# Kernel tuning notes

Hardware: AMD Instinct MI355X
Metric: run time of the kernel (lower is better)

## Reference

```python
import jax, jax.numpy as jnp
import numpy as np

B, S, E, H = 2, 2048, 1024, 16
DK = E // H


def setup_inputs() -> dict:
    key = jax.random.key(0)
    ks = jax.random.split(key, 8)
    scale = 1.0 / np.sqrt(E)
    inp = {
        "query": jax.random.normal(ks[0], (B, S, E), jnp.float32),
        "key": jax.random.normal(ks[1], (B, S, E), jnp.float32),
        "value": jax.random.normal(ks[2], (B, S, E), jnp.float32),
        # causal mask: True = masked out (upper triangle)
        "attn_mask": jnp.triu(jnp.ones((S, S), jnp.bool_), k=1),
        "Wq": jax.random.normal(ks[3], (E, E), jnp.float32) * scale,
        "bq": jnp.zeros((E,), jnp.float32),
        "Wk": jax.random.normal(ks[4], (E, E), jnp.float32) * scale,
        "bk": jnp.zeros((E,), jnp.float32),
        "Wv": jax.random.normal(ks[5], (E, E), jnp.float32) * scale,
        "bv": jnp.zeros((E,), jnp.float32),
        "Wo": jax.random.normal(ks[6], (E, E), jnp.float32) * scale,
        "bo": jnp.zeros((E,), jnp.float32),
    }
    return inp


def reference(query, key, value, attn_mask, Wq, bq, Wk, bk, Wv, bv, Wo, bo):
    bs = query.shape[0]
    # QKV projections, split heads: [B,S,E] -> [B,H,S,DK]
    def proj(x, W, b):
        y = jnp.einsum('bse,ef->bsf', x, W) + b
        return y.reshape(bs, -1, H, DK).transpose(0, 2, 1, 3)

    q = proj(query, Wq, bq)
    k = proj(key, Wk, bk)
    v = proj(value, Wv, bv)

    # scaled dot-product attention with additive -1e9 mask fill
    scores = jnp.einsum('bhqd,bhkd->bhqk', q, k) / np.sqrt(DK).astype(jnp.float32)
    scores = jnp.where(attn_mask[None, None, :, :], jnp.float32(-1e9), scores)
    attn = jax.nn.softmax(scores, axis=-1)
    ctx = jnp.einsum('bhqk,bhkd->bhqd', attn, v)  # [B,H,S,DK]

    concat = ctx.transpose(0, 2, 1, 3).reshape(bs, -1, E)  # [B,S,E]
    return jnp.einsum('bse,ef->bsf', concat, Wo) + bo
```

## Files before the change

### kernel.cpp

```cpp
#include <hip/hip_runtime.h>
#include <hip/hip_bf16.h>

typedef __attribute__((ext_vector_type(8))) short bf16x8;
typedef __attribute__((ext_vector_type(4))) float f32x4;

constexpr int Bc = 2, Sc = 2048, Ec = 1024, Hc = 16, DKc = 64;

__device__ __forceinline__ unsigned short f2b(float f) {
    union { float f; unsigned u; } v; v.f = f;
    unsigned u = v.u;
    return (unsigned short)((u + 0x7FFFu + ((u >> 16) & 1u)) >> 16);
}
__device__ __forceinline__ unsigned short f2bn(float f) {
    return __bfloat16_as_ushort(__float2bfloat16(f));
}
__device__ __forceinline__ float b2f(unsigned short h) {
    union { unsigned u; float f; } v; v.u = ((unsigned)h) << 16;
    return v.f;
}

#define GLOAD16(ldsp, gp)                                                                  \
    __builtin_amdgcn_global_load_lds((const __attribute__((address_space(1))) void*)(gp),  \
                                     (__attribute__((address_space(3))) void*)(ldsp),      \
                                     16, 0, 0)

#define ASM_VM6 asm volatile("s_waitcnt vmcnt(6)" ::: "memory")
#define ASM_VM4 asm volatile("s_waitcnt vmcnt(4)" ::: "memory")
#define ASM_VM0 asm volatile("s_waitcnt vmcnt(0)" ::: "memory")
#define ASM_LG0 asm volatile("s_waitcnt lgkmcnt(0)" ::: "memory")
#define ASM_BAR asm volatile("s_barrier" ::: "memory")

__global__ __launch_bounds__(256) void conv_w(
    const float* __restrict__ Wq, const float* __restrict__ Wk,
    const float* __restrict__ Wv, const float* __restrict__ Wo,
    unsigned short* __restrict__ Wt)
{
    const int z = blockIdx.z;
    const float* W = (z == 0) ? Wq : (z == 1) ? Wk : (z == 2) ? Wv : Wo;
    unsigned short* O = Wt + (size_t)z * 1048576;
    __shared__ unsigned short T[64][65];
    const int k0 = blockIdx.y * 64, n0 = blockIdx.x * 64;
    const int tx = threadIdx.x & 15, ty = threadIdx.x >> 4;
    #pragma unroll
    for (int p = 0; p < 4; p++) {
        float4 v = *(const float4*)&W[(size_t)(k0 + ty + 16 * p) * 1024 + n0 + 4 * tx];
        T[ty + 16 * p][4 * tx + 0] = f2b(v.x);
        T[ty + 16 * p][4 * tx + 1] = f2b(v.y);
        T[ty + 16 * p][4 * tx + 2] = f2b(v.z);
        T[ty + 16 * p][4 * tx + 3] = f2b(v.w);
    }
    __syncthreads();
    #pragma unroll
    for (int p = 0; p < 4; p++) {
        ushort4 o;
        o.x = T[4 * tx + 0][ty + 16 * p];
        o.y = T[4 * tx + 1][ty + 16 * p];
        o.z = T[4 * tx + 2][ty + 16 * p];
        o.w = T[4 * tx + 3][ty + 16 * p];
        *(ushort4*)&O[(size_t)(n0 + ty + 16 * p) * 1024 + k0 + 4 * tx] = o;
    }
}

__global__ __launch_bounds__(256, 2) void gemm_qkv(
    const float* __restrict__ Xq, const float* __restrict__ Xk, const float* __restrict__ Xv,
    const unsigned short* __restrict__ Wt,
    const float* __restrict__ bq, const float* __restrict__ bk, const float* __restrict__ bv,
    unsigned short* __restrict__ Qw, unsigned short* __restrict__ Kw,
    unsigned short* __restrict__ Vt)
{
    const int wgid = blockIdx.x;
    const int xcd = wgid & 7, slot = wgid >> 3;
    const int y = xcd + 8 * (slot & 3);
    const int xz = slot >> 2;
    const int x = xz & 7, z = xz >> 3;

    const float* Ag = (z == 0) ? Xq : (z == 1) ? Xk : Xv;
    const unsigned short* Bg = Wt + (size_t)z * 1048576;
    const float* bias = (z == 0) ? bq : (z == 1) ? bk : bv;

    __shared__ __align__(16) float SA[2][4096];
    __shared__ __align__(16) unsigned short SB[2][4096];

    const int tid = threadIdx.x;
    const int m0 = y * 128, n0 = x * 128;
    const int lane = tid & 63, c = lane & 15, g = lane >> 4;
    const int w = tid >> 6;
    const int wr = (w >> 1) * 64, wc = (w & 1) * 64;
    const int cc = c & 7;
    const int arow = lane >> 3;
    const int achk = ((lane & 7) ^ arow) << 4;
    const int lr = lane >> 2;
    const int lcs = ((lane & 3) ^ ((lane >> 3) & 3)) * 8;

#define QKV_STAGE(buf, kk)                                                                 \
    _Pragma("unroll")                                                                      \
    for (int i = 0; i < 4; i++)                                                            \
        GLOAD16((char*)SA[buf] + i * 4096 + w * 1024,                                      \
                (const char*)Ag + (size_t)(m0 + 32 * i + 8 * w + arow) * 4096 +            \
                (size_t)(kk) * 4 + achk);                                                  \
    _Pragma("unroll")                                                                      \
    for (int i = 0; i < 2; i++) {                                                          \
        const int rb = 32 * w + 16 * i;                                                    \
        GLOAD16(SB[buf] + rb * 32, Bg + (size_t)(n0 + rb + lr) * 1024 + (kk) + lcs);       \
    }

    f32x4 acc[4][4] = {};
    QKV_STAGE(0, 0)
    QKV_STAGE(1, 32)
    for (int t = 0; t < 32; t++) {
        const int cur = t & 1;
        if (t < 31) { ASM_VM6; } else { ASM_VM0; }
        ASM_BAR;
        f32x4 afr[4][2];
        bf16x8 b[4];
        #pragma unroll
        for (int m = 0; m < 4; m++) {
            const char* ab = (const char*)SA[cur] + (wr + 16 * m + c) * 128;
            afr[m][0] = *(const f32x4*)(ab + (((2 * g) ^ cc) << 4));
            afr[m][1] = *(const f32x4*)(ab + (((2 * g + 1) ^ cc) << 4));
        }
        #pragma unroll
        for (int n = 0; n < 4; n++)
            b[n] = *(const bf16x8*)((const char*)SB[cur] +
                   (wc + 16 * n + c) * 64 + ((g ^ ((c >> 1) & 3)) << 4));
        ASM_LG0;
        ASM_BAR;
        if (t + 2 < 32) { QKV_STAGE(cur, (t + 2) * 32) }
        bf16x8 a[4];
        #pragma unroll
        for (int m = 0; m < 4; m++) {
            bf16x8 av;
            av[0] = (short)f2bn(afr[m][0][0]); av[1] = (short)f2bn(afr[m][0][1]);
            av[2] = (short)f2bn(afr[m][0][2]); av[3] = (short)f2bn(afr[m][0][3]);
            av[4] = (short)f2bn(afr[m][1][0]); av[5] = (short)f2bn(afr[m][1][1]);
            av[6] = (short)f2bn(afr[m][1][2]); av[7] = (short)f2bn(afr[m][1][3]);
            a[m] = av;
        }
        __builtin_amdgcn_s_setprio(1);
        #pragma unroll
        for (int m = 0; m < 4; m++)
            #pragma unroll
            for (int n = 0; n < 4; n++)
                acc[m][n] = __builtin_amdgcn_mfma_f32_16x16x32_bf16(a[m], b[n], acc[m][n], 0, 0, 0);
        __builtin_amdgcn_s_setprio(0);
    }
#undef QKV_STAGE

    if (z == 2) {
        unsigned short* Tr = (unsigned short*)&SA[0][0];
        ASM_BAR;
        #pragma unroll
        for (int n = 0; n < 4; n++) {
            const int dl = wc + n * 16 + c;
            const float bv_ = bias[n0 + dl];
            #pragma unroll
            for (int m = 0; m < 4; m++) {
                const int sl = wr + m * 16 + 4 * g;
                ushort4 pw;
                pw.x = f2bn(acc[m][n][0] + bv_);
                pw.y = f2bn(acc[m][n][1] + bv_);
                pw.z = f2bn(acc[m][n][2] + bv_);
                pw.w = f2bn(acc[m][n][3] + bv_);
                const int sc = (sl >> 2) ^ (dl & 7);
                *(ushort4*)&Tr[dl * 128 + sc * 4] = pw;
            }
        }
        ASM_BAR;
        #pragma unroll
        for (int it = 0; it < 16; it++) {
            const int idx = it * 256 + tid;
            const int dl = idx >> 5;
            const int sc0 = idx & 31;
            const int sc = sc0 ^ (dl & 7);
            const ushort4 pw = *(const ushort4*)&Tr[dl * 128 + sc * 4];
            const int gn = n0 + dl;
            const int h = gn >> 6, d = gn & 63;
            const int gm = m0 + sc0 * 4;
            const int bb = gm >> 11, s = gm & 2047;
            *(ushort4*)&Vt[((size_t)(bb * Hc + h) * DKc + d) * Sc + s] = pw;
        }
    } else {
        #pragma unroll
        for (int n = 0; n < 4; n++) {
            const int gn = n0 + wc + n * 16 + c;
            const float bv_ = bias[gn];
            const int h = gn >> 6, d = gn & 63;
            #pragma unroll
            for (int m = 0; m < 4; m++) {
                #pragma unroll
                for (int r = 0; r < 4; r++) {
                    const int gm = m0 + wr + m * 16 + 4 * g + r;
                    const int bb = gm >> 11, s = gm & 2047;
                    const float val = acc[m][n][r] + bv_;
                    if (z == 0)
                        Qw[((size_t)(bb * Hc + h) * Sc + s) * DKc + d] = f2bn(val * 0.125f);
                    else
                        Kw[((size_t)(bb * Hc + h) * Sc + s) * DKc + d] = f2bn(val);
                }
            }
        }
    }
}

__global__ __launch_bounds__(256) void gemm_out(
    const unsigned short* __restrict__ Ctx, const unsigned short* __restrict__ Wt,
    const float* __restrict__ bo, float* __restrict__ Out)
{
    const int wgid = blockIdx.x;
    const int xcd = wgid & 7, slot = wgid >> 3;
    const int y = xcd + 8 * (slot & 3);
    const int x = slot >> 2;

    const unsigned short* Ag = Ctx;
    const unsigned short* Bg = Wt + (size_t)3 * 1048576;

    __shared__ __align__(16) unsigned short SMEM[4][4096];

    const int tid = threadIdx.x;
    const int m0 = y * 128, n0 = x * 128;
    const int lane = tid & 63, c = lane & 15, g = lane >> 4;
    const int w = tid >> 6;
    const int wr = (w >> 1) * 64, wc = (w & 1) * 64;
    const int lr = lane >> 2;
    const int lcs = ((lane & 3) ^ ((lane >> 3) & 3)) * 8;

#define OUT_STAGE(buf, kk)                                                                 \
    _Pragma("unroll")                                                                      \
    for (int i = 0; i < 2; i++) {                                                          \
        const int rb = 32 * w + 16 * i;                                                    \
        GLOAD16(SMEM[buf] + rb * 32, Ag + (size_t)(m0 + rb + lr) * 1024 + (kk) + lcs);     \
        GLOAD16(SMEM[2 + (buf)] + rb * 32, Bg + (size_t)(n0 + rb + lr) * 1024 + (kk) + lcs); \
    }

    f32x4 acc[4][4] = {};
    OUT_STAGE(0, 0)
    OUT_STAGE(1, 32)
    for (int t = 0; t < 32; t++) {
        const int cur = t & 1;
        if (t < 31) { ASM_VM4; } else { ASM_VM0; }
        ASM_BAR;
        bf16x8 a[4], b[4];
        #pragma unroll
        for (int m = 0; m < 4; m++)
            a[m] = *(const bf16x8*)((const char*)SMEM[cur] +
                   (wr + 16 * m + c) * 64 + ((g ^ ((c >> 1) & 3)) << 4));
        #pragma unroll
        for (int n = 0; n < 4; n++)
            b[n] = *(const bf16x8*)((const char*)SMEM[2 + cur] +
                   (wc + 16 * n + c) * 64 + ((g ^ ((c >> 1) & 3)) << 4));
        ASM_LG0;
        ASM_BAR;
        if (t + 2 < 32) { OUT_STAGE(cur, (t + 2) * 32) }
        __builtin_amdgcn_s_setprio(1);
        #pragma unroll
        for (int m = 0; m < 4; m++)
            #pragma unroll
            for (int n = 0; n < 4; n++)
                acc[m][n] = __builtin_amdgcn_mfma_f32_16x16x32_bf16(a[m], b[n], acc[m][n], 0, 0, 0);
        __builtin_amdgcn_s_setprio(0);
    }
#undef OUT_STAGE

    #pragma unroll
    for (int n = 0; n < 4; n++) {
        const int gn = n0 + wc + n * 16 + c;
        const float bv_ = bo[gn];
        #pragma unroll
        for (int m = 0; m < 4; m++) {
            #pragma unroll
            for (int r = 0; r < 4; r++) {
                const int gm = m0 + wr + m * 16 + 4 * g + r;
                Out[(size_t)gm * Ec + gn] = acc[m][n][r] + bv_;
            }
        }
    }
}

__global__ __launch_bounds__(256) void attn(
    const unsigned short* __restrict__ Qw, const unsigned short* __restrict__ Kw,
    const unsigned short* __restrict__ Vt,
    unsigned short* __restrict__ Opart, float* __restrict__ Lpart)
{
    const int bid = blockIdx.x;
    const int bh = bid & 31;
    const int ps = bid >> 5;
    const int pair = ps >> 1, sp = ps & 1;
    const int tid = threadIdx.x, w = tid >> 6, lane = tid & 63;
    const int c = lane & 15, g = lane >> 4;

    const unsigned short* Qh = Qw + (size_t)bh * Sc * DKc;
    const unsigned short* Kh = Kw + (size_t)bh * Sc * DKc;
    const unsigned short* Vh = Vt + (size_t)bh * DKc * Sc;

    __shared__ __align__(16) unsigned short Kl[4096];
    __shared__ __align__(16) unsigned short Vl[4096];
    __shared__ __align__(16) unsigned short Pl[4][16][72];

    const int lrow8 = lane >> 3;
    const int cbp = ((lane & 7) ^ lrow8) << 4;
    const int swz = (c & 7) << 4;

#define STAGE_KV(KV0)                                                                       \
    _Pragma("unroll")                                                                       \
    for (int s2 = 0; s2 < 2; s2++) {                                                        \
        const int row_ = s2 * 32 + w * 8 + lrow8;                                           \
        GLOAD16((char*)Kl + s2 * 4096 + w * 1024,                                           \
                (const char*)Kh + (size_t)((KV0) + row_) * 128 + cbp);                      \
        GLOAD16((char*)Vl + s2 * 4096 + w * 1024,                                           \
                (const char*)Vh + (size_t)row_ * 4096 + (size_t)(KV0) * 2 + cbp);           \
    }

    for (int half = 0; half < 2; half++) {
        const int qt = half ? (31 - pair) : pair;
        const int qbase = qt * 64;
        const int qrow = qbase + w * 16 + c;
        const int qtg = bh * 32 + qt;

        const bf16x8 q0 = *(const bf16x8*)&Qh[(size_t)qrow * DKc + 8 * g];
        const bf16x8 q1 = *(const bf16x8*)&Qh[(size_t)qrow * DKc + 32 + 8 * g];

        float lsum = 0.f;
        f32x4 o[4] = {};

        for (int j = sp; j <= qt; j += 2) {
            const int kv0 = j * 64;
            const bool maskt = (j == qt);

            STAGE_KV(kv0)
            __syncthreads();

            f32x4 d[4] = {};
            __builtin_amdgcn_s_setprio(1);
            #pragma unroll
            for (int t = 0; t < 4; t++) {
                const char* kb = (const char*)Kl + (16 * t + c) * 128;
                const bf16x8 k0 = *(const bf16x8*)(kb + ((16 * g) ^ swz));
                const bf16x8 k1 = *(const bf16x8*)(kb + ((64 + 16 * g) ^ swz));
                d[t] = __builtin_amdgcn_mfma_f32_16x16x32_bf16(k0, q0, d[t], 0, 0, 0);
                d[t] = __builtin_amdgcn_mfma_f32_16x16x32_bf16(k1, q1, d[t], 0, 0, 0);
            }
            __builtin_amdgcn_s_setprio(0);

            float s[16];
            if (maskt) {
                #pragma unroll
                for (int t = 0; t < 4; t++)
                    #pragma unroll
                    for (int r = 0; r < 4; r++) {
                        const int kv = kv0 + 16 * t + 4 * g + r;
                        s[4 * t + r] = __expf((kv <= qrow) ? d[t][r] : -1e30f);
                    }
            } else {
                #pragma unroll
                for (int t = 0; t < 4; t++)
                    #pragma unroll
                    for (int r = 0; r < 4; r++)
                        s[4 * t + r] = __expf(d[t][r]);
            }
            #pragma unroll
            for (int i = 0; i < 16; i++) lsum += s[i];

            #pragma unroll
            for (int t = 0; t < 4; t++) {
                ushort4 pw;
                pw.x = f2bn(s[4 * t + 0]); pw.y = f2bn(s[4 * t + 1]);
                pw.z = f2bn(s[4 * t + 2]); pw.w = f2bn(s[4 * t + 3]);
                *(ushort4*)&Pl[w][c][16 * t + 4 * g] = pw;
            }
            const bf16x8 pA0 = *(const bf16x8*)&Pl[w][c][8 * g];
            const bf16x8 pA1 = *(const bf16x8*)&Pl[w][c][32 + 8 * g];

            __builtin_amdgcn_s_setprio(1);
            #pragma unroll
            for (int ch = 0; ch < 4; ch++) {
                const char* vb = (const char*)Vl + (16 * ch + c) * 128;
                const bf16x8 v0 = *(const bf16x8*)(vb + ((16 * g) ^ swz));
                const bf16x8 v1 = *(const bf16x8*)(vb + ((64 + 16 * g) ^ swz));
                f32x4 t = o[ch];
                t = __builtin_amdgcn_mfma_f32_16x16x32_bf16(pA0, v0, t, 0, 0, 0);
                o[ch] = __builtin_amdgcn_mfma_f32_16x16x32_bf16(pA1, v1, t, 0, 0, 0);
            }
            __builtin_amdgcn_s_setprio(0);
            __syncthreads();
        }

        lsum += __shfl_xor(lsum, 16);
        lsum += __shfl_xor(lsum, 32);
        if (g == 0)
            Lpart[((size_t)sp * 1024 + qtg) * 64 + w * 16 + c] = lsum;

        #pragma unroll
        for (int ch = 0; ch < 4; ch++) {
            #pragma unroll
            for (int r = 0; r < 4; r++) {
                const int lrow = w * 16 + 4 * g + r;
                Opart[(((size_t)sp * 1024 + qtg) * 64 + lrow) * 64 + ch * 16 + c] =
                    f2bn(o[ch][r]);
            }
        }
    }
#undef STAGE_KV
}

__global__ __launch_bounds__(256) void attn_combine(
    const unsigned short* __restrict__ Opart, const float* __restrict__ Lpart,
    unsigned short* __restrict__ Ctx)
{
    const int qtg = blockIdx.x;
    const int bh = qtg >> 5, qt = qtg & 31;
    const int bb = bh >> 4, hh = bh & 15;
    #pragma unroll
    for (int it = 0; it < 2; it++) {
        const int chunk = threadIdx.x + it * 256;
        const int row = chunk >> 3, c8 = (chunk & 7) * 8;
        const size_t o0 = ((size_t)qtg * 64 + row) * 64 + c8;
        const size_t o1 = ((size_t)(1024 + qtg) * 64 + row) * 64 + c8;
        const bf16x8 a = *(const bf16x8*)&Opart[o0];
        const bf16x8 b = *(const bf16x8*)&Opart[o1];
        const float linv = 1.f / (Lpart[(size_t)qtg * 64 + row] +
                                  Lpart[(size_t)(1024 + qtg) * 64 + row]);
        ushort4 lo, hi;
        lo.x = f2bn((b2f((unsigned short)a[0]) + b2f((unsigned short)b[0])) * linv);
        lo.y = f2bn((b2f((unsigned short)a[1]) + b2f((unsigned short)b[1])) * linv);
        lo.z = f2bn((b2f((unsigned short)a[2]) + b2f((unsigned short)b[2])) * linv);
        lo.w = f2bn((b2f((unsigned short)a[3]) + b2f((unsigned short)b[3])) * linv);
        hi.x = f2bn((b2f((unsigned short)a[4]) + b2f((unsigned short)b[4])) * linv);
        hi.y = f2bn((b2f((unsigned short)a[5]) + b2f((unsigned short)b[5])) * linv);
        hi.z = f2bn((b2f((unsigned short)a[6]) + b2f((unsigned short)b[6])) * linv);
        hi.w = f2bn((b2f((unsigned short)a[7]) + b2f((unsigned short)b[7])) * linv);
        const int qg = qt * 64 + row;
        unsigned short* dst = &Ctx[((size_t)(bb * Sc + qg)) * Ec + hh * 64 + c8];
        *(ushort4*)dst = lo;
        *(ushort4*)(dst + 4) = hi;
    }
}

extern "C" void kernel_launch(void* const* d_in, const int* in_sizes, int n_in,
                              void* d_out, int out_size, void* d_ws, size_t ws_size,
                              hipStream_t stream) {
    const float* query = (const float*)d_in[0];
    const float* key   = (const float*)d_in[1];
    const float* value = (const float*)d_in[2];
    const float* Wq = (const float*)d_in[4];
    const float* bq = (const float*)d_in[5];
    const float* Wk = (const float*)d_in[6];
    const float* bk = (const float*)d_in[7];
    const float* Wv = (const float*)d_in[8];
    const float* bv = (const float*)d_in[9];
    const float* Wo = (const float*)d_in[10];
    const float* bo = (const float*)d_in[11];

    const size_t n_elem = (size_t)Bc * Hc * Sc * DKc;
    unsigned short* Qw = (unsigned short*)d_ws;
    unsigned short* Kw = Qw + n_elem;
    unsigned short* Vt = Kw + n_elem;
    unsigned short* Cx = Vt + n_elem;
    unsigned short* Sp = Cx + n_elem;
    unsigned short* Wt = Sp + 3 * n_elem;

    unsigned short* Opart = Sp;
    float* Lpart = (float*)(Sp + (size_t)2 * 1024 * 64 * 64);

    conv_w<<<dim3(16, 16, 4), 256, 0, stream>>>(Wq, Wk, Wv, Wo, Wt);
    gemm_qkv<<<dim3(768), 256, 0, stream>>>(query, key, value, Wt, bq, bk, bv, Qw, Kw, Vt);
    attn<<<dim3(1024), 256, 0, stream>>>(Qw, Kw, Vt, Opart, Lpart);
    attn_combine<<<dim3(1024), 256, 0, stream>>>(Opart, Lpart, Cx);
    gemm_out<<<dim3(256), 256, 0, stream>>>(Cx, Wt, bo, (float*)d_out);
}
```

Measured before the change: 101.1 us.

## Pre-convert activations to bf16 and use 256x256 tiles in QKV GEMM

Adds a conv_x kernel that converts the fp32 query/key/value inputs to bf16 in a workspace before the projection GEMM. The QKV GEMM then loads bf16 A tiles directly, with no per-iteration fp32-to-bf16 conversion, and is restructured to 512 threads with 256x256 output tiles (192 blocks instead of 768) for more operand reuse. The trade is an extra full pass over the inputs (read fp32, write bf16) and fewer, larger blocks on a 256-CU device. It also raises per-thread accumulator pressure with 8x4 MFMA tiles per wave.

```diff
diff --git a/kernel.cpp b/kernel.cpp
--- a/kernel.cpp
+++ b/kernel.cpp
@@ -24,11 +24,25 @@
                                      (__attribute__((address_space(3))) void*)(ldsp),      \
                                      16, 0, 0)
 
-#define ASM_VM6 asm volatile("s_waitcnt vmcnt(6)" ::: "memory")
 #define ASM_VM4 asm volatile("s_waitcnt vmcnt(4)" ::: "memory")
 #define ASM_VM0 asm volatile("s_waitcnt vmcnt(0)" ::: "memory")
 #define ASM_LG0 asm volatile("s_waitcnt lgkmcnt(0)" ::: "memory")
 #define ASM_BAR asm volatile("s_barrier" ::: "memory")
+
+__global__ __launch_bounds__(256) void conv_x(
+    const float* __restrict__ Xq, const float* __restrict__ Xk, const float* __restrict__ Xv,
+    unsigned short* __restrict__ Xb)
+{
+    const int z = blockIdx.y;
+    const float* X = (z == 0) ? Xq : (z == 1) ? Xk : Xv;
+    unsigned short* O = Xb + (size_t)z * 4194304;
+    const int n4 = 4194304 / 4;
+    for (int i = blockIdx.x * 256 + threadIdx.x; i < n4; i += gridDim.x * 256) {
+        float4 v = ((const float4*)X)[i];
+        ushort4 h; h.x = f2b(v.x); h.y = f2b(v.y); h.z = f2b(v.z); h.w = f2b(v.w);
+        ((ushort4*)O)[i] = h;
+    }
+}
 
 __global__ __launch_bounds__(256) void conv_w(
     const float* __restrict__ Wq, const float* __restrict__ Wk,
@@ -61,84 +75,67 @@
     }
 }
 
-__global__ __launch_bounds__(256, 2) void gemm_qkv(
-    const float* __restrict__ Xq, const float* __restrict__ Xk, const float* __restrict__ Xv,
-    const unsigned short* __restrict__ Wt,
+__global__ __launch_bounds__(512, 2) void gemm_qkv(
+    const unsigned short* __restrict__ Xb, const unsigned short* __restrict__ Wt,
     const float* __restrict__ bq, const float* __restrict__ bk, const float* __restrict__ bv,
     unsigned short* __restrict__ Qw, unsigned short* __restrict__ Kw,
     unsigned short* __restrict__ Vt)
 {
     const int wgid = blockIdx.x;
-    const int xcd = wgid & 7, slot = wgid >> 3;
-    const int y = xcd + 8 * (slot & 3);
-    const int xz = slot >> 2;
-    const int x = xz & 7, z = xz >> 3;
-
-    const float* Ag = (z == 0) ? Xq : (z == 1) ? Xk : Xv;
+    const int xcd = wgid & 7;
+    const int s = wgid >> 3;
+    const int z = s >> 3;
+    const int t8 = s & 7;
+    const int nb = t8 >> 1;
+    const int mb = (t8 & 1) * 8 + xcd;
+
+    const unsigned short* Ag = Xb + (size_t)z * 4194304;
     const unsigned short* Bg = Wt + (size_t)z * 1048576;
     const float* bias = (z == 0) ? bq : (z == 1) ? bk : bv;
 
-    __shared__ __align__(16) float SA[2][4096];
-    __shared__ __align__(16) unsigned short SB[2][4096];
+    __shared__ __align__(16) unsigned short SMEM[32768];
 
     const int tid = threadIdx.x;
-    const int m0 = y * 128, n0 = x * 128;
+    const int m0 = mb * 256, n0 = nb * 256;
     const int lane = tid & 63, c = lane & 15, g = lane >> 4;
     const int w = tid >> 6;
-    const int wr = (w >> 1) * 64, wc = (w & 1) * 64;
-    const int cc = c & 7;
-    const int arow = lane >> 3;
-    const int achk = ((lane & 7) ^ arow) << 4;
-    const int lr = lane >> 2;
+    const int wr = w >> 2;
+    const int wc = w & 3;
     const int lcs = ((lane & 3) ^ ((lane >> 3) & 3)) * 8;
+    const int rowin = (lane >> 2);
 
 #define QKV_STAGE(buf, kk)                                                                 \
     _Pragma("unroll")                                                                      \
-    for (int i = 0; i < 4; i++)                                                            \
-        GLOAD16((char*)SA[buf] + i * 4096 + w * 1024,                                      \
-                (const char*)Ag + (size_t)(m0 + 32 * i + 8 * w + arow) * 4096 +            \
-                (size_t)(kk) * 4 + achk);                                                  \
-    _Pragma("unroll")                                                                      \
-    for (int i = 0; i < 2; i++) {                                                          \
-        const int rb = 32 * w + 16 * i;                                                    \
-        GLOAD16(SB[buf] + rb * 32, Bg + (size_t)(n0 + rb + lr) * 1024 + (kk) + lcs);       \
-    }
-
-    f32x4 acc[4][4] = {};
+    for (int r2 = 0; r2 < 2; r2++) {                                                       \
+        GLOAD16((char*)SMEM + (buf) * 16384 + r2 * 8192 + w * 1024,                        \
+                Ag + (size_t)(m0 + r2 * 128 + w * 16 + rowin) * 1024 + (kk) + lcs);        \
+        GLOAD16((char*)SMEM + 32768 + (buf) * 16384 + r2 * 8192 + w * 1024,                \
+                Bg + (size_t)(n0 + r2 * 128 + w * 16 + rowin) * 1024 + (kk) + lcs);        \
+    }
+
+    f32x4 acc[8][4] = {};
     QKV_STAGE(0, 0)
     QKV_STAGE(1, 32)
     for (int t = 0; t < 32; t++) {
         const int cur = t & 1;
-        if (t < 31) { ASM_VM6; } else { ASM_VM0; }
+        if (t < 31) { ASM_VM4; } else { ASM_VM0; }
         ASM_BAR;
-        f32x4 afr[4][2];
-        bf16x8 b[4];
-        #pragma unroll
-        for (int m = 0; m < 4; m++) {
-            const char* ab = (const char*)SA[cur] + (wr + 16 * m + c) * 128;
-            afr[m][0] = *(const f32x4*)(ab + (((2 * g) ^ cc) << 4));
-            afr[m][1] = *(const f32x4*)(ab + (((2 * g + 1) ^ cc) << 4));
-        }
+        bf16x8 a[8], b[4];
+        const int rchk = (g ^ ((c >> 1) & 3)) << 4;
+        #pragma unroll
+        for (int m = 0; m < 8; m++)
+            a[m] = *(const bf16x8*)((const char*)SMEM + cur * 16384 +
+                                    (wr * 128 + m * 16 + c) * 64 + rchk);
         #pragma unroll
         for (int n = 0; n < 4; n++)
-            b[n] = *(const bf16x8*)((const char*)SB[cur] +
-                   (wc + 16 * n + c) * 64 + ((g ^ ((c >> 1) & 3)) << 4));
+            b[n] = *(const bf16x8*)((const char*)SMEM + 32768 + cur * 16384 +
+                                    (wc * 64 + n * 16 + c) * 64 + rchk);
         ASM_LG0;
         ASM_BAR;
         if (t + 2 < 32) { QKV_STAGE(cur, (t + 2) * 32) }
-        bf16x8 a[4];
-        #pragma unroll
-        for (int m = 0; m < 4; m++) {
-            bf16x8 av;
-            av[0] = (short)f2bn(afr[m][0][0]); av[1] = (short)f2bn(afr[m][0][1]);
-            av[2] = (short)f2bn(afr[m][0][2]); av[3] = (short)f2bn(afr[m][0][3]);
-            av[4] = (short)f2bn(afr[m][1][0]); av[5] = (short)f2bn(afr[m][1][1]);
-            av[6] = (short)f2bn(afr[m][1][2]); av[7] = (short)f2bn(afr[m][1][3]);
-            a[m] = av;
-        }
         __builtin_amdgcn_s_setprio(1);
         #pragma unroll
-        for (int m = 0; m < 4; m++)
+        for (int m = 0; m < 8; m++)
             #pragma unroll
             for (int n = 0; n < 4; n++)
                 acc[m][n] = __builtin_amdgcn_mfma_f32_16x16x32_bf16(a[m], b[n], acc[m][n], 0, 0, 0);
@@ -147,55 +144,60 @@
 #undef QKV_STAGE
 
     if (z == 2) {
-        unsigned short* Tr = (unsigned short*)&SA[0][0];
-        ASM_BAR;
-        #pragma unroll
-        for (int n = 0; n < 4; n++) {
-            const int dl = wc + n * 16 + c;
-            const float bv_ = bias[n0 + dl];
-            #pragma unroll
-            for (int m = 0; m < 4; m++) {
-                const int sl = wr + m * 16 + 4 * g;
-                ushort4 pw;
-                pw.x = f2bn(acc[m][n][0] + bv_);
-                pw.y = f2bn(acc[m][n][1] + bv_);
-                pw.z = f2bn(acc[m][n][2] + bv_);
-                pw.w = f2bn(acc[m][n][3] + bv_);
-                const int sc = (sl >> 2) ^ (dl & 7);
-                *(ushort4*)&Tr[dl * 128 + sc * 4] = pw;
-            }
-        }
-        ASM_BAR;
-        #pragma unroll
-        for (int it = 0; it < 16; it++) {
-            const int idx = it * 256 + tid;
-            const int dl = idx >> 5;
-            const int sc0 = idx & 31;
-            const int sc = sc0 ^ (dl & 7);
-            const ushort4 pw = *(const ushort4*)&Tr[dl * 128 + sc * 4];
-            const int gn = n0 + dl;
-            const int h = gn >> 6, d = gn & 63;
-            const int gm = m0 + sc0 * 4;
-            const int bb = gm >> 11, s = gm & 2047;
-            *(ushort4*)&Vt[((size_t)(bb * Hc + h) * DKc + d) * Sc + s] = pw;
+        unsigned short* Tr = SMEM;
+        #pragma unroll
+        for (int p = 0; p < 2; p++) {
+            ASM_BAR;
+            if ((wc >> 1) == p) {
+                #pragma unroll
+                for (int n = 0; n < 4; n++) {
+                    const int dl = (wc & 1) * 64 + n * 16 + c;
+                    const float bv_ = bias[n0 + p * 128 + dl];
+                    #pragma unroll
+                    for (int m = 0; m < 8; m++) {
+                        const int sl = wr * 128 + m * 16 + 4 * g;
+                        ushort4 pw;
+                        pw.x = f2bn(acc[m][n][0] + bv_);
+                        pw.y = f2bn(acc[m][n][1] + bv_);
+                        pw.z = f2bn(acc[m][n][2] + bv_);
+                        pw.w = f2bn(acc[m][n][3] + bv_);
+                        const int sc = (sl >> 2) ^ (dl & 7);
+                        *(ushort4*)&Tr[dl * 256 + sc * 4] = pw;
+                    }
+                }
+            }
+            ASM_BAR;
+            #pragma unroll
+            for (int it = 0; it < 16; it++) {
+                const int idx = it * 512 + tid;
+                const int dl = idx >> 6;
+                const int sc0 = idx & 63;
+                const int sc = sc0 ^ (dl & 7);
+                const ushort4 pw = *(const ushort4*)&Tr[dl * 256 + sc * 4];
+                const int gn = n0 + p * 128 + dl;
+                const int h = gn >> 6, d = gn & 63;
+                const int gm = m0 + sc0 * 4;
+                const int bb = gm >> 11, ss = gm & 2047;
+                *(ushort4*)&Vt[((size_t)(bb * Hc + h) * DKc + d) * Sc + ss] = pw;
+            }
         }
     } else {
         #pragma unroll
         for (int n = 0; n < 4; n++) {
-            const int gn = n0 + wc + n * 16 + c;
+            const int gn = n0 + wc * 64 + n * 16 + c;
             const float bv_ = bias[gn];
             const int h = gn >> 6, d = gn & 63;
             #pragma unroll
-            for (int m = 0; m < 4; m++) {
+            for (int m = 0; m < 8; m++) {
                 #pragma unroll
                 for (int r = 0; r < 4; r++) {
-                    const int gm = m0 + wr + m * 16 + 4 * g + r;
-                    const int bb = gm >> 11, s = gm & 2047;
+                    const int gm = m0 + wr * 128 + m * 16 + 4 * g + r;
+                    const int bb = gm >> 11, ss = gm & 2047;
                     const float val = acc[m][n][r] + bv_;
                     if (z == 0)
-                        Qw[((size_t)(bb * Hc + h) * Sc + s) * DKc + d] = f2bn(val * 0.125f);
+                        Qw[((size_t)(bb * Hc + h) * Sc + ss) * DKc + d] = f2bn(val * 0.125f);
                     else
-                        Kw[((size_t)(bb * Hc + h) * Sc + s) * DKc + d] = f2bn(val);
+                        Kw[((size_t)(bb * Hc + h) * Sc + ss) * DKc + d] = f2bn(val);
                 }
             }
         }
@@ -455,14 +457,15 @@
     unsigned short* Kw = Qw + n_elem;
     unsigned short* Vt = Kw + n_elem;
     unsigned short* Cx = Vt + n_elem;
-    unsigned short* Sp = Cx + n_elem;
-    unsigned short* Wt = Sp + 3 * n_elem;
-
-    unsigned short* Opart = Sp;
-    float* Lpart = (float*)(Sp + (size_t)2 * 1024 * 64 * 64);
-
+    unsigned short* Xb = Cx + n_elem;
+    unsigned short* Wt = Xb + 3 * n_elem;
+
+    unsigned short* Opart = Xb;
+    float* Lpart = (float*)(Xb + (size_t)2 * 1024 * 64 * 64);
+
+    conv_x<<<dim3(512, 3), 256, 0, stream>>>(query, key, value, Xb);
     conv_w<<<dim3(16, 16, 4), 256, 0, stream>>>(Wq, Wk, Wv, Wo, Wt);
-    gemm_qkv<<<dim3(768), 256, 0, stream>>>(query, key, value, Wt, bq, bk, bv, Qw, Kw, Vt);
+    gemm_qkv<<<dim3(192), 512, 0, stream>>>(Xb, Wt, bq, bk, bv, Qw, Kw, Vt);
     attn<<<dim3(1024), 256, 0, stream>>>(Qw, Kw, Vt, Opart, Lpart);
     attn_combine<<<dim3(1024), 256, 0, stream>>>(Opart, Lpart, Cx);
     gemm_out<<<dim3(256), 256, 0, stream>>>(Cx, Wt, bo, (float*)d_out);
```

Result: slower. 107.8 us (+6.6%).

## Load fp32 A tiles to registers and store bf16 to LDS in QKV GEMM

Applied to the files above, without the earlier changes.

The QKV projection GEMM used to copy fp32 activation tiles straight into LDS with async global-to-LDS loads, then convert them to bf16 after every LDS read. Now A tiles are loaded into registers, converted to bf16 once, and written into a bf16 LDS buffer one stage ahead, while B keeps the async LDS path. This halves A's LDS footprint and read traffic and removes repeated conversion work. In exchange it adds register pressure, since the launch-bounds occupancy hint was dropped and the loop fully unrolled, and it relies on hand-tuned vmcnt waits that must match the issue order.

```diff
diff --git a/kernel.cpp b/kernel.cpp
--- a/kernel.cpp
+++ b/kernel.cpp
@@ -24,8 +24,10 @@
                                      (__attribute__((address_space(3))) void*)(ldsp),      \
                                      16, 0, 0)
 
+#define ASM_VM8 asm volatile("s_waitcnt vmcnt(8)" ::: "memory")
 #define ASM_VM6 asm volatile("s_waitcnt vmcnt(6)" ::: "memory")
 #define ASM_VM4 asm volatile("s_waitcnt vmcnt(4)" ::: "memory")
+#define ASM_VM2 asm volatile("s_waitcnt vmcnt(2)" ::: "memory")
 #define ASM_VM0 asm volatile("s_waitcnt vmcnt(0)" ::: "memory")
 #define ASM_LG0 asm volatile("s_waitcnt lgkmcnt(0)" ::: "memory")
 #define ASM_BAR asm volatile("s_barrier" ::: "memory")
@@ -61,7 +63,7 @@
     }
 }
 
-__global__ __launch_bounds__(256, 2) void gemm_qkv(
+__global__ __launch_bounds__(256) void gemm_qkv(
     const float* __restrict__ Xq, const float* __restrict__ Xk, const float* __restrict__ Xv,
     const unsigned short* __restrict__ Wt,
     const float* __restrict__ bq, const float* __restrict__ bk, const float* __restrict__ bv,
@@ -78,63 +80,69 @@
     const unsigned short* Bg = Wt + (size_t)z * 1048576;
     const float* bias = (z == 0) ? bq : (z == 1) ? bk : bv;
 
-    __shared__ __align__(16) float SA[2][4096];
-    __shared__ __align__(16) unsigned short SB[2][4096];
+    __shared__ __align__(16) unsigned short SMEM[16384];
 
     const int tid = threadIdx.x;
     const int m0 = y * 128, n0 = x * 128;
     const int lane = tid & 63, c = lane & 15, g = lane >> 4;
     const int w = tid >> 6;
     const int wr = (w >> 1) * 64, wc = (w & 1) * 64;
-    const int cc = c & 7;
-    const int arow = lane >> 3;
-    const int achk = ((lane & 7) ^ arow) << 4;
     const int lr = lane >> 2;
     const int lcs = ((lane & 3) ^ ((lane >> 3) & 3)) * 8;
 
-#define QKV_STAGE(buf, kk)                                                                 \
-    _Pragma("unroll")                                                                      \
-    for (int i = 0; i < 4; i++)                                                            \
-        GLOAD16((char*)SA[buf] + i * 4096 + w * 1024,                                      \
-                (const char*)Ag + (size_t)(m0 + 32 * i + 8 * w + arow) * 4096 +            \
-                (size_t)(kk) * 4 + achk);                                                  \
+#define LDA(RS, kt)                                                                        \
+    RS[0] = *(const float4*)&Ag[(size_t)(m0 + 32 * w + lr) * 1024 + (kt) * 32 + lcs];      \
+    RS[1] = *(const float4*)&Ag[(size_t)(m0 + 32 * w + lr) * 1024 + (kt) * 32 + lcs + 4];  \
+    RS[2] = *(const float4*)&Ag[(size_t)(m0 + 32 * w + 16 + lr) * 1024 + (kt) * 32 + lcs]; \
+    RS[3] = *(const float4*)&Ag[(size_t)(m0 + 32 * w + 16 + lr) * 1024 + (kt) * 32 + lcs + 4];
+#define LDB(buf, kt)                                                                       \
     _Pragma("unroll")                                                                      \
     for (int i = 0; i < 2; i++) {                                                          \
         const int rb = 32 * w + 16 * i;                                                    \
-        GLOAD16(SB[buf] + rb * 32, Bg + (size_t)(n0 + rb + lr) * 1024 + (kk) + lcs);       \
+        GLOAD16(SMEM + 8192 + (buf) * 4096 + rb * 32,                                      \
+                Bg + (size_t)(n0 + rb + lr) * 1024 + (kt) * 32 + lcs);                     \
+    }
+#define WRA(RS, buf)                                                                       \
+    _Pragma("unroll")                                                                      \
+    for (int i = 0; i < 2; i++) {                                                          \
+        bf16x8 pk;                                                                         \
+        pk[0] = (short)f2bn(RS[2 * i].x);     pk[1] = (short)f2bn(RS[2 * i].y);            \
+        pk[2] = (short)f2bn(RS[2 * i].z);     pk[3] = (short)f2bn(RS[2 * i].w);            \
+        pk[4] = (short)f2bn(RS[2 * i + 1].x); pk[5] = (short)f2bn(RS[2 * i + 1].y);        \
+        pk[6] = (short)f2bn(RS[2 * i + 1].z); pk[7] = (short)f2bn(RS[2 * i + 1].w);        \
+        *(bf16x8*)(SMEM + (buf) * 4096 + (32 * w + 16 * i + lr) * 32 + (lane & 3) * 8) = pk; \
     }
 
     f32x4 acc[4][4] = {};
-    QKV_STAGE(0, 0)
-    QKV_STAGE(1, 32)
+    float4 rAe[4], rAo[4];
+
+    LDA(rAe, 0)
+    LDB(0, 0)
+    ASM_VM2;
+    WRA(rAe, 0)
+    LDA(rAo, 1)
+    LDB(1, 1)
+    ASM_LG0;
+
+    #pragma unroll
     for (int t = 0; t < 32; t++) {
         const int cur = t & 1;
         if (t < 31) { ASM_VM6; } else { ASM_VM0; }
         ASM_BAR;
-        f32x4 afr[4][2];
-        bf16x8 b[4];
-        #pragma unroll
-        for (int m = 0; m < 4; m++) {
-            const char* ab = (const char*)SA[cur] + (wr + 16 * m + c) * 128;
-            afr[m][0] = *(const f32x4*)(ab + (((2 * g) ^ cc) << 4));
-            afr[m][1] = *(const f32x4*)(ab + (((2 * g + 1) ^ cc) << 4));
-        }
+        bf16x8 a[4], b[4];
+        #pragma unroll
+        for (int m = 0; m < 4; m++)
+            a[m] = *(const bf16x8*)((const char*)SMEM + cur * 8192 +
+                   (wr + 16 * m + c) * 64 + ((g ^ ((c >> 1) & 3)) << 4));
         #pragma unroll
         for (int n = 0; n < 4; n++)
-            b[n] = *(const bf16x8*)((const char*)SB[cur] +
+            b[n] = *(const bf16x8*)((const char*)SMEM + 16384 + cur * 8192 +
                    (wc + 16 * n + c) * 64 + ((g ^ ((c >> 1) & 3)) << 4));
         ASM_LG0;
         ASM_BAR;
-        if (t + 2 < 32) { QKV_STAGE(cur, (t + 2) * 32) }
-        bf16x8 a[4];
-        #pragma unroll
-        for (int m = 0; m < 4; m++) {
-            bf16x8 av;
-            av[0] = (short)f2bn(afr[m][0][0]); av[1] = (short)f2bn(afr[m][0][1]);
-            av[2] = (short)f2bn(afr[m][0][2]); av[3] = (short)f2bn(afr[m][0][3]);
-            av[4] = (short)f2bn(afr[m][1][0]); av[5] = (short)f2bn(afr[m][1][1]);
-            av[6] = (short)f2bn(afr[m][1][2]); av[7] = (short)f2bn(afr[m][1][3]);
-            a[m] = av;
+        if (t + 2 < 32) {
+            if ((t & 1) == 0) { LDA(rAe, t + 2) } else { LDA(rAo, t + 2) }
+            LDB(cur, t + 2)
         }
         __builtin_amdgcn_s_setprio(1);
         #pragma unroll
@@ -143,11 +151,18 @@
             for (int n = 0; n < 4; n++)
                 acc[m][n] = __builtin_amdgcn_mfma_f32_16x16x32_bf16(a[m], b[n], acc[m][n], 0, 0, 0);
         __builtin_amdgcn_s_setprio(0);
-    }
-#undef QKV_STAGE
+        if (t + 1 < 32) {
+            if (t + 2 < 32) { ASM_VM8; } else { ASM_VM2; }
+            if ((t & 1) == 0) { WRA(rAo, cur ^ 1) } else { WRA(rAe, cur ^ 1) }
+        }
+        ASM_LG0;
+    }
+#undef LDA
+#undef LDB
+#undef WRA
 
     if (z == 2) {
-        unsigned short* Tr = (unsigned short*)&SA[0][0];
+        unsigned short* Tr = SMEM;
         ASM_BAR;
         #pragma unroll
         for (int n = 0; n < 4; n++) {
```

Measured after the change: 125.5 us. 1.24x slower.

## Share staged KV tiles between paired causal query tiles in one loop

Applied to the files above, without the earlier changes.

Rather than processing the two paired query tiles (pair and 31-pair) one after the other, each staging its own KV tiles, the kernel now walks the KV range once for the longer tile. Each staged K/V tile is used for both query tiles while the shorter one still needs it. This roughly halves KV global-to-LDS traffic and the barriers for the shared prefix. In exchange it holds two sets of accumulators and Q fragments in registers, which may raise register pressure and lower occupancy. The shared Pl scratch buffer is reused by both tiles within one iteration.

```diff
diff --git a/kernel.cpp b/kernel.cpp
--- a/kernel.cpp
+++ b/kernel.cpp
@@ -310,96 +310,103 @@
                 (const char*)Vh + (size_t)row_ * 4096 + (size_t)(KV0) * 2 + cbp);           \
     }
 
-    for (int half = 0; half < 2; half++) {
-        const int qt = half ? (31 - pair) : pair;
-        const int qbase = qt * 64;
-        const int qrow = qbase + w * 16 + c;
-        const int qtg = bh * 32 + qt;
-
-        const bf16x8 q0 = *(const bf16x8*)&Qh[(size_t)qrow * DKc + 8 * g];
-        const bf16x8 q1 = *(const bf16x8*)&Qh[(size_t)qrow * DKc + 32 + 8 * g];
-
-        float lsum = 0.f;
-        f32x4 o[4] = {};
-
-        for (int j = sp; j <= qt; j += 2) {
-            const int kv0 = j * 64;
-            const bool maskt = (j == qt);
-
-            STAGE_KV(kv0)
-            __syncthreads();
-
-            f32x4 d[4] = {};
-            __builtin_amdgcn_s_setprio(1);
-            #pragma unroll
-            for (int t = 0; t < 4; t++) {
-                const char* kb = (const char*)Kl + (16 * t + c) * 128;
-                const bf16x8 k0 = *(const bf16x8*)(kb + ((16 * g) ^ swz));
-                const bf16x8 k1 = *(const bf16x8*)(kb + ((64 + 16 * g) ^ swz));
-                d[t] = __builtin_amdgcn_mfma_f32_16x16x32_bf16(k0, q0, d[t], 0, 0, 0);
-                d[t] = __builtin_amdgcn_mfma_f32_16x16x32_bf16(k1, q1, d[t], 0, 0, 0);
-            }
-            __builtin_amdgcn_s_setprio(0);
-
-            float s[16];
-            if (maskt) {
-                #pragma unroll
-                for (int t = 0; t < 4; t++)
-                    #pragma unroll
-                    for (int r = 0; r < 4; r++) {
-                        const int kv = kv0 + 16 * t + 4 * g + r;
-                        s[4 * t + r] = __expf((kv <= qrow) ? d[t][r] : -1e30f);
-                    }
-            } else {
-                #pragma unroll
-                for (int t = 0; t < 4; t++)
-                    #pragma unroll
-                    for (int r = 0; r < 4; r++)
-                        s[4 * t + r] = __expf(d[t][r]);
-            }
-            #pragma unroll
-            for (int i = 0; i < 16; i++) lsum += s[i];
-
-            #pragma unroll
-            for (int t = 0; t < 4; t++) {
-                ushort4 pw;
-                pw.x = f2bn(s[4 * t + 0]); pw.y = f2bn(s[4 * t + 1]);
-                pw.z = f2bn(s[4 * t + 2]); pw.w = f2bn(s[4 * t + 3]);
-                *(ushort4*)&Pl[w][c][16 * t + 4 * g] = pw;
-            }
-            const bf16x8 pA0 = *(const bf16x8*)&Pl[w][c][8 * g];
-            const bf16x8 pA1 = *(const bf16x8*)&Pl[w][c][32 + 8 * g];
-
-            __builtin_amdgcn_s_setprio(1);
-            #pragma unroll
-            for (int ch = 0; ch < 4; ch++) {
-                const char* vb = (const char*)Vl + (16 * ch + c) * 128;
-                const bf16x8 v0 = *(const bf16x8*)(vb + ((16 * g) ^ swz));
-                const bf16x8 v1 = *(const bf16x8*)(vb + ((64 + 16 * g) ^ swz));
-                f32x4 t = o[ch];
-                t = __builtin_amdgcn_mfma_f32_16x16x32_bf16(pA0, v0, t, 0, 0, 0);
-                o[ch] = __builtin_amdgcn_mfma_f32_16x16x32_bf16(pA1, v1, t, 0, 0, 0);
-            }
-            __builtin_amdgcn_s_setprio(0);
-            __syncthreads();
-        }
-
-        lsum += __shfl_xor(lsum, 16);
-        lsum += __shfl_xor(lsum, 32);
-        if (g == 0)
-            Lpart[((size_t)sp * 1024 + qtg) * 64 + w * 16 + c] = lsum;
-
-        #pragma unroll
-        for (int ch = 0; ch < 4; ch++) {
-            #pragma unroll
-            for (int r = 0; r < 4; r++) {
-                const int lrow = w * 16 + 4 * g + r;
-                Opart[(((size_t)sp * 1024 + qtg) * 64 + lrow) * 64 + ch * 16 + c] =
-                    f2bn(o[ch][r]);
-            }
+#define QKPV(Q0, Q1, QT, QROW, LSUM, OACC, J, KV0)                                          \
+    {                                                                                       \
+        f32x4 d[4] = {};                                                                    \
+        __builtin_amdgcn_s_setprio(1);                                                      \
+        _Pragma("unroll")                                                                   \
+        for (int t = 0; t < 4; t++) {                                                       \
+            const char* kb = (const char*)Kl + (16 * t + c) * 128;                          \
+            const bf16x8 k0 = *(const bf16x8*)(kb + ((16 * g) ^ swz));                      \
+            const bf16x8 k1 = *(const bf16x8*)(kb + ((64 + 16 * g) ^ swz));                 \
+            d[t] = __builtin_amdgcn_mfma_f32_16x16x32_bf16(k0, Q0, d[t], 0, 0, 0);          \
+            d[t] = __builtin_amdgcn_mfma_f32_16x16x32_bf16(k1, Q1, d[t], 0, 0, 0);          \
+        }                                                                                   \
+        __builtin_amdgcn_s_setprio(0);                                                      \
+        float s[16];                                                                        \
+        if ((J) == (QT)) {                                                                  \
+            _Pragma("unroll")                                                               \
+            for (int t = 0; t < 4; t++)                                                     \
+                _Pragma("unroll")                                                           \
+                for (int r = 0; r < 4; r++) {                                               \
+                    const int kv = (KV0) + 16 * t + 4 * g + r;                              \
+                    s[4 * t + r] = __expf((kv <= (QROW)) ? d[t][r] : -1e30f);               \
+                }                                                                           \
+        } else {                                                                            \
+            _Pragma("unroll")                                                               \
+            for (int t = 0; t < 4; t++)                                                     \
+                _Pragma("unroll")                                                           \
+                for (int r = 0; r < 4; r++)                                                 \
+                    s[4 * t + r] = __expf(d[t][r]);                                         \
+        }                                                                                   \
+        _Pragma("unroll")                                                                   \
+        for (int i = 0; i < 16; i++) LSUM += s[i];                                          \
+        _Pragma("unroll")                                                                   \
+        for (int t = 0; t < 4; t++) {                                                       \
+            ushort4 pw;                                                                     \
+            pw.x = f2bn(s[4 * t + 0]); pw.y = f2bn(s[4 * t + 1]);                           \
+            pw.z = f2bn(s[4 * t + 2]); pw.w = f2bn(s[4 * t + 3]);                           \
+            *(ushort4*)&Pl[w][c][16 * t + 4 * g] = pw;                                      \
+        }                                                                                   \
+        const bf16x8 pA0 = *(const bf16x8*)&Pl[w][c][8 * g];                                \
+        const bf16x8 pA1 = *(const bf16x8*)&Pl[w][c][32 + 8 * g];                           \
+        __builtin_amdgcn_s_setprio(1);                                                      \
+        _Pragma("unroll")                                                                   \
+        for (int ch = 0; ch < 4; ch++) {                                                    \
+            const char* vb = (const char*)Vl + (16 * ch + c) * 128;                         \
+            const bf16x8 v0 = *(const bf16x8*)(vb + ((16 * g) ^ swz));                      \
+            const bf16x8 v1 = *(const bf16x8*)(vb + ((64 + 16 * g) ^ swz));                 \
+            f32x4 tacc = OACC[ch];                                                          \
+            tacc = __builtin_amdgcn_mfma_f32_16x16x32_bf16(pA0, v0, tacc, 0, 0, 0);         \
+            OACC[ch] = __builtin_amdgcn_mfma_f32_16x16x32_bf16(pA1, v1, tacc, 0, 0, 0);     \
+        }                                                                                   \
+        __builtin_amdgcn_s_setprio(0);                                                      \
+    }
+
+    const int qtA = pair, qtB = 31 - pair;
+    const int qrowA = qtA * 64 + w * 16 + c;
+    const int qrowB = qtB * 64 + w * 16 + c;
+
+    const bf16x8 qA0 = *(const bf16x8*)&Qh[(size_t)qrowA * DKc + 8 * g];
+    const bf16x8 qA1 = *(const bf16x8*)&Qh[(size_t)qrowA * DKc + 32 + 8 * g];
+    const bf16x8 qB0 = *(const bf16x8*)&Qh[(size_t)qrowB * DKc + 8 * g];
+    const bf16x8 qB1 = *(const bf16x8*)&Qh[(size_t)qrowB * DKc + 32 + 8 * g];
+
+    float lsumA = 0.f, lsumB = 0.f;
+    f32x4 oA[4] = {}, oB[4] = {};
+
+    for (int j = sp; j <= qtB; j += 2) {
+        const int kv0 = j * 64;
+        STAGE_KV(kv0)
+        __syncthreads();
+        QKPV(qB0, qB1, qtB, qrowB, lsumB, oB, j, kv0)
+        if (j <= qtA) { QKPV(qA0, qA1, qtA, qrowA, lsumA, oA, j, kv0) }
+        __syncthreads();
+    }
+
+    lsumA += __shfl_xor(lsumA, 16);
+    lsumA += __shfl_xor(lsumA, 32);
+    lsumB += __shfl_xor(lsumB, 16);
+    lsumB += __shfl_xor(lsumB, 32);
+    const int qtgA = bh * 32 + qtA;
+    const int qtgB = bh * 32 + qtB;
+    if (g == 0) {
+        Lpart[((size_t)sp * 1024 + qtgA) * 64 + w * 16 + c] = lsumA;
+        Lpart[((size_t)sp * 1024 + qtgB) * 64 + w * 16 + c] = lsumB;
+    }
+    #pragma unroll
+    for (int ch = 0; ch < 4; ch++) {
+        #pragma unroll
+        for (int r = 0; r < 4; r++) {
+            const int lrow = w * 16 + 4 * g + r;
+            Opart[(((size_t)sp * 1024 + qtgA) * 64 + lrow) * 64 + ch * 16 + c] =
+                f2bn(oA[ch][r]);
+            Opart[(((size_t)sp * 1024 + qtgB) * 64 + lrow) * 64 + ch * 16 + c] =
+                f2bn(oB[ch][r]);
         }
     }
 #undef STAGE_KV
+#undef QKPV
 }
 
 __global__ __launch_bounds__(256) void attn_combine(
```

New measurement: 109.1 us. 1.08x slower.
